# Optimization experiments

Measured on AMD Instinct MI355X. Metric: run time of the kernel, lower is better.

The kernel has to match this reference:

```python
import jax, jax.numpy as jnp
from jax import lax
import numpy as np

B, S, H, L = 128, 256, 768, 24


def setup_inputs() -> dict:
    key = jax.random.key(0)
    k_tf, k_len, k_w, k_tr, k_st, k_en = jax.random.split(key, 6)
    token_features = jax.random.normal(k_tf, (B, S, H), dtype=jnp.float32)
    # contiguous valid lengths in [3, S] (>=3 so that stripping CLS/SEP leaves >=1 token)
    lengths = jax.random.randint(k_len, (B,), 3, S + 1)
    pos = jnp.arange(S)
    input_mask = (pos[None, :] < lengths[:, None]).astype(jnp.int32)
    true_label_mask = (pos[None, :] < (lengths - 2)[:, None]).astype(jnp.int32)
    W = jax.random.normal(k_w, (H, L), dtype=jnp.float32) * 0.02
    b = jnp.zeros((L,), dtype=jnp.float32)
    transitions = jax.random.normal(k_tr, (L, L), dtype=jnp.float32) * 0.1
    start_trans = jax.random.normal(k_st, (L,), dtype=jnp.float32) * 0.1
    end_trans = jax.random.normal(k_en, (L,), dtype=jnp.float32) * 0.1
    return {
        "token_features": token_features,
        "input_mask": input_mask,
        "true_label_mask": true_label_mask,
        "W": W,
        "b": b,
        "transitions": transitions,
        "start_trans": start_trans,
        "end_trans": end_trans,
    }


def _compact(x, mask):
    """Vectorized version of the torch per-token copy loop: for each row,
    gather valid tokens (mask==1) preserving order, drop the first and last
    valid token (CLS/SEP), left-pack into a zero tensor."""
    # stable argsort puts valid positions first, in order
    order = jnp.argsort(1 - mask.astype(jnp.int32), axis=1)  # [B,S]
    gathered = jnp.take_along_axis(x, order[:, :, None], axis=1)  # [B,S,H]
    # drop first valid token (shift left by 1), pad a zero row at the end
    shifted = jnp.concatenate([gathered[:, 1:], jnp.zeros_like(gathered[:, :1])], axis=1)
    n_valid = mask.sum(axis=1)  # [B]
    keep = jnp.arange(x.shape[1])[None, :] < (n_valid[:, None] - 2)  # also drops last (SEP)
    return jnp.where(keep[:, :, None], shifted, 0.0)


def _viterbi(emissions, mask, transitions, start_trans, end_trans):
    """Masked Viterbi decode. emissions [B,S,L], mask [B,S] bool."""
    Bn, Sn, Ln = emissions.shape
    lbl = jnp.arange(Ln)
    score0 = start_trans[None, :] + emissions[:, 0]  # [B,L]

    def step(score, xs):
        em_t, m_t = xs  # [B,L], [B]
        cand = score[:, :, None] + transitions[None]  # [B,prev,curr]
        best = cand.max(axis=1) + em_t
        bp = cand.argmax(axis=1)  # [B,L] best prev tag per curr tag
        new_score = jnp.where(m_t[:, None], best, score)
        bp = jnp.where(m_t[:, None], bp, lbl[None, :])  # identity backpointer on pad
        return new_score, bp

    ems = jnp.swapaxes(emissions[:, 1:], 0, 1)  # [S-1,B,L]
    ms = jnp.swapaxes(mask[:, 1:], 0, 1)  # [S-1,B]
    final, bps = lax.scan(step, score0, (ems, ms))
    final = final + end_trans[None, :]
    best_score = final.max(axis=1)  # [B]
    last_tag = final.argmax(axis=1)  # [B]

    def back(tag, bp):  # tag: tag at time t; bp: bp_t -> tag at t-1
        prev = jnp.take_along_axis(bp, tag[:, None], axis=1)[:, 0]
        return prev, tag

    tag0, tags_rest = lax.scan(back, last_tag, bps, reverse=True)  # tags_rest [S-1,B]
    path = jnp.concatenate([tag0[:, None], jnp.swapaxes(tags_rest, 0, 1)], axis=1)  # [B,S]
    return best_score, path


def reference(token_features, input_mask, true_label_mask, W, b, transitions, start_trans, end_trans):
    mask = input_mask.astype(bool)
    wv = _compact(token_features, mask)  # dropout is identity at inference
    emissions = jax.nn.sigmoid(wv @ W + b)  # [B,S,L]
    _, path = _viterbi(emissions, true_label_mask != 0, transitions, start_trans, end_trans)
    return path
```

## Files before the change

kernel.cpp:

```cpp
#include <hip/hip_runtime.h>
#include <hip/hip_bf16.h>
#include <math.h>

#define NB 128
#define NS 256
#define NH 768
#define NL 24
#define ASTR 68

__global__ __launch_bounds__(256) void ner_emis(
    const float* __restrict__ tf, const int* __restrict__ tlm,
    const float* __restrict__ W, const float* __restrict__ bias,
    float* __restrict__ E)
{
    const int b    = blockIdx.x >> 3;
    const int tile = (blockIdx.x & 7) << 5;
    const int tid  = threadIdx.x;
    if (tlm[b*NS + tile] == 0) return;

    __shared__ float lds[8*32*25];
    float* As = lds;
    float* Ws = lds + 32*ASTR;
    float* Pr = lds;

    const int tok  = tid & 15;
    const int ksub = tid >> 4;
    const int kk   = ksub << 2;
    const int rot  = ksub & 3;

    float acc0[NL], acc1[NL];
    #pragma unroll
    for (int l = 0; l < NL; ++l) { acc0[l] = 0.f; acc1[l] = 0.f; }

    const float* tfb = tf + (size_t)(b*NS)*NH;

    for (int kc0 = 0; kc0 < NH; kc0 += 64) {
        #pragma unroll
        for (int i = 0; i < 2; ++i) {
            int idx  = tid + (i << 8);
            int row  = idx >> 4;
            int c4   = idx & 15;
            int trow = tile + row + 1;
            if (trow > 255) trow = 255;
            float4 v = *(const float4*)(tfb + (size_t)trow*NH + kc0 + (c4 << 2));
            float* dst = As + row*ASTR + (c4 << 2);
            dst[0] = v.x; dst[1] = v.y; dst[2] = v.z; dst[3] = v.w;
        }
        {
            const float4* wsrc = (const float4*)(W + (size_t)kc0*NL);
            float4* wdst = (float4*)Ws;
            for (int i = tid; i < 384; i += 256) wdst[i] = wsrc[i];
        }
        __syncthreads();

        const float* A0 = As + tok*ASTR + kk;
        const float* A1 = A0 + 16*ASTR;
        const float* Wr = Ws + kk*NL;
        #pragma unroll
        for (int s = 0; s < 4; ++s) {
            const int j = (s + rot) & 3;
            float a0 = A0[j];
            float a1 = A1[j];
            const float4* w4 = (const float4*)(Wr + j*NL);
            float wv[NL];
            #pragma unroll
            for (int i = 0; i < 6; ++i) {
                float4 w = w4[i];
                wv[4*i+0] = w.x; wv[4*i+1] = w.y; wv[4*i+2] = w.z; wv[4*i+3] = w.w;
            }
            #pragma unroll
            for (int l = 0; l < NL; ++l) {
                acc0[l] = fmaf(a0, wv[l], acc0[l]);
                acc1[l] = fmaf(a1, wv[l], acc1[l]);
            }
        }
        __syncthreads();
    }

    if (ksub >= 8) {
        float* p = Pr + ((ksub-8)*32 + tok)*25;
        float* q = p + 16*25;
        #pragma unroll
        for (int l = 0; l < NL; ++l) { p[l] = acc0[l]; q[l] = acc1[l]; }
    }
    __syncthreads();
    if (ksub < 8) {
        const float* p = Pr + (ksub*32 + tok)*25;
        const float* q = p + 16*25;
        #pragma unroll
        for (int l = 0; l < NL; ++l) { acc0[l] += p[l]; acc1[l] += q[l]; }
    }
    __syncthreads();
    if (ksub < 8) {
        float* p = Pr + (ksub*32 + tok)*25;
        float* q = p + 16*25;
        #pragma unroll
        for (int l = 0; l < NL; ++l) { p[l] = acc0[l]; q[l] = acc1[l]; }
    }
    __syncthreads();

    const int* tm = tlm + b*NS + tile;
    float* Eb = E + (size_t)(b*NS + tile)*NL;
    #pragma unroll
    for (int i = 0; i < 3; ++i) {
        int o = tid + (i << 8);
        int t = o / NL, l = o % NL;
        if (tm[t]) {
            float s = 0.f;
            #pragma unroll
            for (int ks = 0; ks < 8; ++ks)
                s += Pr[(ks*32 + t)*25 + l];
            float x = s + bias[l];
            Eb[t*NL + l] = 1.0f/(1.0f + expf(-x));
        }
    }
}

__global__ __launch_bounds__(256) void ner_viterbi(
    const float* __restrict__ E, const int* __restrict__ tlm,
    const float* __restrict__ trans, const float* __restrict__ st,
    const float* __restrict__ en, int* __restrict__ out)
{
    const int tid = threadIdx.x;
    const int b   = blockIdx.x;
    const int bS  = b*NS;

    __shared__ float Esh[NS*NL];
    __shared__ float scl[NS*NL];
    __shared__ float Tt[NL*NL];
    __shared__ float fin[NL];
    __shared__ unsigned char tr_s[NL][NS];
    __shared__ int chosen[12];
    __shared__ int nsh, ltag;

    {
        const float4* src = (const float4*)(E + (size_t)bS*NL);
        float4* dst = (float4*)Esh;
        #pragma unroll
        for (int j = 0; j < 6; ++j) dst[tid + (j << 8)] = src[tid + (j << 8)];
    }
    for (int i = tid; i < NL*NL; i += 256) {
        int c = i / NL, p = i % NL;
        Tt[i] = trans[p*NL + c];
    }
    if (tid < 64) {
        int a = tlm[bS+tid] + tlm[bS+tid+64] + tlm[bS+tid+128] + tlm[bS+tid+192];
        #pragma unroll
        for (int off = 32; off > 0; off >>= 1) a += __shfl_down(a, off, 64);
        if (tid == 0) nsh = a;
    }
    __syncthreads();
    const int n = nsh;

    if (tid < 64) {
        const int c = tid % 24;
        float Tc[24];
        #pragma unroll
        for (int p = 0; p < 24; ++p) Tc[p] = trans[p*NL + c];

        auto rl = [](float v, int p) {
            return __int_as_float(__builtin_amdgcn_readlane(__float_as_int(v), p));
        };

        float sv = st[c] + Esh[c];
        scl[c] = sv;
        float scr[24];
        #pragma unroll
        for (int p = 0; p < 24; ++p) scr[p] = rl(sv, p);

        auto step = [&](int t, float em) {
            float cand[24];
            #pragma unroll
            for (int p = 0; p < 24; ++p) cand[p] = scr[p] + Tc[p];
            float m0 = fmaxf(fmaxf(cand[0],  cand[1]),  cand[2]);
            float m1 = fmaxf(fmaxf(cand[3],  cand[4]),  cand[5]);
            float m2 = fmaxf(fmaxf(cand[6],  cand[7]),  cand[8]);
            float m3 = fmaxf(fmaxf(cand[9],  cand[10]), cand[11]);
            float m4 = fmaxf(fmaxf(cand[12], cand[13]), cand[14]);
            float m5 = fmaxf(fmaxf(cand[15], cand[16]), cand[17]);
            float m6 = fmaxf(fmaxf(cand[18], cand[19]), cand[20]);
            float m7 = fmaxf(fmaxf(cand[21], cand[22]), cand[23]);
            float q0 = fmaxf(fmaxf(m0, m1), m2);
            float q1 = fmaxf(fmaxf(m3, m4), m5);
            float q2 = fmaxf(m6, m7);
            float best = fmaxf(fmaxf(q0, q1), q2);
            sv = best + em;
            scl[t*NL + c] = sv;
            #pragma unroll
            for (int p = 0; p < 24; ++p) scr[p] = rl(sv, p);
        };

        int t = 1;
        for (; t + 8 <= n; t += 8) {
            float em[8];
            const float* eb = Esh + t*NL + c;
            #pragma unroll
            for (int j = 0; j < 8; ++j) em[j] = eb[j*NL];
            #pragma unroll
            for (int j = 0; j < 8; ++j) step(t + j, em[j]);
        }
        for (; t < n; ++t) step(t, Esh[t*NL + c]);
        fin[c] = sv + en[c];
    }
    __syncthreads();

    if (tid == 0) {
        float bv = fin[0]; int bt = 0;
        #pragma unroll
        for (int cc = 1; cc < 24; ++cc) { if (fin[cc] > bv) { bv = fin[cc]; bt = cc; } }
        ltag = bt;
    }
    __syncthreads();

    const int K = (n > 1) ? (n - 1 + 9) / 10 : 1;
    if (n > 1 && tid < 240) {
        const int w = tid / 24 + 1, h = tid % 24;
        int tlo = (w-1)*K; if (tlo > n-1) tlo = n-1;
        int thi = w*K;     if (thi > n-1) thi = n-1;
        int cur = h;
        for (int t = thi; t > tlo; --t) {
            const float4* sp = (const float4*)(scl + (t-1)*NL);
            const float4* up = (const float4*)(Tt  + cur*NL);
            float cand[24];
            #pragma unroll
            for (int i = 0; i < 6; ++i) {
                float4 s = sp[i], u = up[i];
                cand[4*i+0] = s.x + u.x;
                cand[4*i+1] = s.y + u.y;
                cand[4*i+2] = s.z + u.z;
                cand[4*i+3] = s.w + u.w;
            }
            float best = cand[0]; int arg = 0;
            #pragma unroll
            for (int p = 1; p < 24; ++p) { if (cand[p] > best) { best = cand[p]; arg = p; } }
            tr_s[h][t-1] = (unsigned char)arg;
            cur = arg;
        }
    }
    __syncthreads();

    if (tid == 0) {
        int cur = ltag;
        for (int w = 10; w >= 1; --w) {
            chosen[w] = cur;
            int tlo = (w-1)*K; if (tlo > n-1) tlo = n-1;
            int thi = w*K;     if (thi > n-1) thi = n-1;
            if (thi > tlo) cur = tr_s[cur][tlo];
        }
    }
    __syncthreads();

    {
        const int t = tid;
        int tag;
        if (t >= n-1) tag = ltag;
        else { int w = t / K + 1; tag = tr_s[chosen[w]][t]; }
        out[bS + t] = tag;
    }
}

extern "C" void kernel_launch(void* const* d_in, const int* in_sizes, int n_in,
                              void* d_out, int out_size, void* d_ws, size_t ws_size,
                              hipStream_t stream) {
    const float* tf    = (const float*)d_in[0];
    const int*   tlm   = (const int*)  d_in[2];
    const float* W     = (const float*)d_in[3];
    const float* bias  = (const float*)d_in[4];
    const float* trans = (const float*)d_in[5];
    const float* st    = (const float*)d_in[6];
    const float* en    = (const float*)d_in[7];
    float* E = (float*)d_ws;

    ner_emis<<<dim3(NB*8), dim3(256), 0, stream>>>(tf, tlm, W, bias, E);
    ner_viterbi<<<dim3(NB), dim3(256), 0, stream>>>(E, tlm, trans, st, en, (int*)d_out);
}
```

Before: 207.5 us.

## Pack two batch rows per wavefront in Viterbi forward pass using ds_bpermute

The Viterbi kernel now handles two batch rows per block, one in each 32-lane half of a single wavefront. Score broadcasts switch from readlane to ds_bpermute, and emissions are prefetched from global memory instead of first being staged into LDS. The backtrace uses 5 windows per row instead of 10, and only 64 blocks are launched. This is meant to halve the number of serial forward recurrences, at the cost of bpermute latency and both rows running to the longer length.

```diff
diff --git a/kernel.cpp b/kernel.cpp
--- a/kernel.cpp
+++ b/kernel.cpp
@@ -7,6 +7,7 @@
 #define NH 768
 #define NL 24
 #define ASTR 68
+#define NW 5
 
 __global__ __launch_bounds__(256) void ner_emis(
     const float* __restrict__ tf, const int* __restrict__ tlm,
@@ -122,56 +123,60 @@
     const float* __restrict__ en, int* __restrict__ out)
 {
     const int tid = threadIdx.x;
-    const int b   = blockIdx.x;
-    const int bS  = b*NS;
-
-    __shared__ float Esh[NS*NL];
-    __shared__ float scl[NS*NL];
+    const int pb  = blockIdx.x;
+
+    __shared__ float scl[2*NS*NL];
     __shared__ float Tt[NL*NL];
-    __shared__ float fin[NL];
-    __shared__ unsigned char tr_s[NL][NS];
-    __shared__ int chosen[12];
-    __shared__ int nsh, ltag;
-
-    {
-        const float4* src = (const float4*)(E + (size_t)bS*NL);
-        float4* dst = (float4*)Esh;
-        #pragma unroll
-        for (int j = 0; j < 6; ++j) dst[tid + (j << 8)] = src[tid + (j << 8)];
-    }
+    __shared__ float fin_s[2*NL];
+    __shared__ unsigned char tr_s[2][NL][NS];
+    __shared__ int chosen_s[2][NW+1];
+    __shared__ int nsh[2], ltag[2];
+
     for (int i = tid; i < NL*NL; i += 256) {
         int c = i / NL, p = i % NL;
         Tt[i] = trans[p*NL + c];
     }
+    if (tid < 128) {
+        const int wv = tid >> 6, ln = tid & 63;
+        const int bb = 2*pb + wv;
+        int a = tlm[bb*NS+ln] + tlm[bb*NS+ln+64] + tlm[bb*NS+ln+128] + tlm[bb*NS+ln+192];
+        #pragma unroll
+        for (int off = 32; off > 0; off >>= 1) a += __shfl_down(a, off, 64);
+        if (ln == 0) nsh[wv] = a;
+    }
+    __syncthreads();
+    const int nA = nsh[0], nB = nsh[1];
+    const int nmax = __builtin_amdgcn_readfirstlane(nA > nB ? nA : nB);
+
     if (tid < 64) {
-        int a = tlm[bS+tid] + tlm[bS+tid+64] + tlm[bS+tid+128] + tlm[bS+tid+192];
-        #pragma unroll
-        for (int off = 32; off > 0; off >>= 1) a += __shfl_down(a, off, 64);
-        if (tid == 0) nsh = a;
-    }
-    __syncthreads();
-    const int n = nsh;
-
-    if (tid < 64) {
-        const int c = tid % 24;
-        float Tc[24];
-        #pragma unroll
-        for (int p = 0; p < 24; ++p) Tc[p] = trans[p*NL + c];
-
-        auto rl = [](float v, int p) {
-            return __int_as_float(__builtin_amdgcn_readlane(__float_as_int(v), p));
+        const int lane  = tid;
+        const int half  = lane >> 5;
+        const int c     = lane & 31;
+        const int cef   = (c < 24) ? c : 23;
+        const bool valid = (c < 24);
+        const int myb   = 2*pb + half;
+        const int hbase = half << 7;
+        const int nh    = half ? nB : nA;
+
+        float Tc[NL];
+        #pragma unroll
+        for (int p = 0; p < NL; ++p) Tc[p] = trans[p*NL + cef];
+
+        const float* Eb = E + (size_t)(myb*NS)*NL + cef;
+        float* sbase = scl + (half*NS)*NL;
+
+        float sv = st[cef] + Eb[0];
+        if (valid) sbase[c] = sv;
+
+        auto bperm = [](int idx, float v) {
+            return __int_as_float(__builtin_amdgcn_ds_bpermute(idx, __float_as_int(v)));
         };
 
-        float sv = st[c] + Esh[c];
-        scl[c] = sv;
-        float scr[24];
-        #pragma unroll
-        for (int p = 0; p < 24; ++p) scr[p] = rl(sv, p);
-
         auto step = [&](int t, float em) {
-            float cand[24];
-            #pragma unroll
-            for (int p = 0; p < 24; ++p) cand[p] = scr[p] + Tc[p];
+            float cand[NL];
+            #pragma unroll
+            for (int p = 0; p < NL; ++p)
+                cand[p] = bperm(hbase + 4*p, sv) + Tc[p];
             float m0 = fmaxf(fmaxf(cand[0],  cand[1]),  cand[2]);
             float m1 = fmaxf(fmaxf(cand[3],  cand[4]),  cand[5]);
             float m2 = fmaxf(fmaxf(cand[6],  cand[7]),  cand[8]);
@@ -184,78 +189,105 @@
             float q1 = fmaxf(fmaxf(m3, m4), m5);
             float q2 = fmaxf(m6, m7);
             float best = fmaxf(fmaxf(q0, q1), q2);
-            sv = best + em;
-            scl[t*NL + c] = sv;
-            #pragma unroll
-            for (int p = 0; p < 24; ++p) scr[p] = rl(sv, p);
+            float nsv = best + em;
+            sv = (t < nh) ? nsv : sv;
+            if (valid) sbase[t*NL + c] = sv;
         };
 
-        int t = 1;
-        for (; t + 8 <= n; t += 8) {
-            float em[8];
-            const float* eb = Esh + t*NL + c;
-            #pragma unroll
-            for (int j = 0; j < 8; ++j) em[j] = eb[j*NL];
-            #pragma unroll
-            for (int j = 0; j < 8; ++j) step(t + j, em[j]);
-        }
-        for (; t < n; ++t) step(t, Esh[t*NL + c]);
-        fin[c] = sv + en[c];
-    }
-    __syncthreads();
-
-    if (tid == 0) {
-        float bv = fin[0]; int bt = 0;
-        #pragma unroll
-        for (int cc = 1; cc < 24; ++cc) { if (fin[cc] > bv) { bv = fin[cc]; bt = cc; } }
-        ltag = bt;
-    }
-    __syncthreads();
-
-    const int K = (n > 1) ? (n - 1 + 9) / 10 : 1;
-    if (n > 1 && tid < 240) {
-        const int w = tid / 24 + 1, h = tid % 24;
-        int tlo = (w-1)*K; if (tlo > n-1) tlo = n-1;
-        int thi = w*K;     if (thi > n-1) thi = n-1;
-        int cur = h;
-        for (int t = thi; t > tlo; --t) {
-            const float4* sp = (const float4*)(scl + (t-1)*NL);
-            const float4* up = (const float4*)(Tt  + cur*NL);
-            float cand[24];
-            #pragma unroll
-            for (int i = 0; i < 6; ++i) {
-                float4 s = sp[i], u = up[i];
-                cand[4*i+0] = s.x + u.x;
-                cand[4*i+1] = s.y + u.y;
-                cand[4*i+2] = s.z + u.z;
-                cand[4*i+3] = s.w + u.w;
-            }
-            float best = cand[0]; int arg = 0;
-            #pragma unroll
-            for (int p = 1; p < 24; ++p) { if (cand[p] > best) { best = cand[p]; arg = p; } }
-            tr_s[h][t-1] = (unsigned char)arg;
-            cur = arg;
-        }
-    }
-    __syncthreads();
-
-    if (tid == 0) {
-        int cur = ltag;
-        for (int w = 10; w >= 1; --w) {
-            chosen[w] = cur;
+        float emb[8];
+        #pragma unroll
+        for (int j = 0; j < 8; ++j) {
+            int tp = 1 + j; if (tp > NS-1) tp = NS-1;
+            emb[j] = Eb[(size_t)tp*NL];
+        }
+        for (int t0 = 1; t0 < nmax; t0 += 8) {
+            float emc[8];
+            #pragma unroll
+            for (int j = 0; j < 8; ++j) emc[j] = emb[j];
+            #pragma unroll
+            for (int j = 0; j < 8; ++j) {
+                int tp = t0 + 8 + j; if (tp > NS-1) tp = NS-1;
+                emb[j] = Eb[(size_t)tp*NL];
+            }
+            #pragma unroll
+            for (int j = 0; j < 8; ++j) {
+                int t = t0 + j;
+                if (t >= nmax) break;
+                step(t, emc[j]);
+            }
+        }
+        if (valid) fin_s[half*NL + c] = sv + en[cef];
+    }
+    __syncthreads();
+
+    if (tid < 2) {
+        const float* f = fin_s + tid*NL;
+        float bv = f[0]; int bt = 0;
+        #pragma unroll
+        for (int cc = 1; cc < 24; ++cc) { if (f[cc] > bv) { bv = f[cc]; bt = cc; } }
+        ltag[tid] = bt;
+    }
+    __syncthreads();
+
+    if (tid < 2*NW*24) {
+        int g = tid;
+        const int bb = g / (NW*24); g -= bb*NW*24;
+        const int w  = g / 24 + 1;
+        const int h  = g % 24;
+        const int n  = nsh[bb];
+        if (n > 1) {
+            const int K = (n - 1 + NW - 1) / NW;
             int tlo = (w-1)*K; if (tlo > n-1) tlo = n-1;
             int thi = w*K;     if (thi > n-1) thi = n-1;
-            if (thi > tlo) cur = tr_s[cur][tlo];
+            const float* sbase = scl + (bb*NS)*NL;
+            int cur = h;
+            for (int t = thi; t > tlo; --t) {
+                const float4* sp = (const float4*)(sbase + (t-1)*NL);
+                const float4* up = (const float4*)(Tt + cur*NL);
+                float cand[NL];
+                #pragma unroll
+                for (int i = 0; i < 6; ++i) {
+                    float4 s = sp[i], u = up[i];
+                    cand[4*i+0] = s.x + u.x;
+                    cand[4*i+1] = s.y + u.y;
+                    cand[4*i+2] = s.z + u.z;
+                    cand[4*i+3] = s.w + u.w;
+                }
+                float best = cand[0]; int arg = 0;
+                #pragma unroll
+                for (int p = 1; p < 24; ++p) { if (cand[p] > best) { best = cand[p]; arg = p; } }
+                tr_s[bb][h][t-1] = (unsigned char)arg;
+                cur = arg;
+            }
+        }
+    }
+    __syncthreads();
+
+    if (tid < 2) {
+        const int bb = tid;
+        const int n  = nsh[bb];
+        const int K  = (n > 1) ? (n - 1 + NW - 1) / NW : 1;
+        int cur = ltag[bb];
+        for (int w = NW; w >= 1; --w) {
+            chosen_s[bb][w] = cur;
+            int tlo = (w-1)*K; if (tlo > n-1) tlo = n-1;
+            int thi = w*K;     if (thi > n-1) thi = n-1;
+            if (thi > tlo) cur = tr_s[bb][cur][tlo];
         }
     }
     __syncthreads();
 
     {
         const int t = tid;
-        int tag;
-        if (t >= n-1) tag = ltag;
-        else { int w = t / K + 1; tag = tr_s[chosen[w]][t]; }
-        out[bS + t] = tag;
+        #pragma unroll
+        for (int bb = 0; bb < 2; ++bb) {
+            const int n = nsh[bb];
+            const int K = (n > 1) ? (n - 1 + NW - 1) / NW : 1;
+            int tag;
+            if (t >= n-1) tag = ltag[bb];
+            else { int w = t / K + 1; tag = tr_s[bb][chosen_s[bb][w]][t]; }
+            out[(2*pb + bb)*NS + t] = tag;
+        }
     }
 }
 
@@ -272,5 +304,5 @@
     float* E = (float*)d_ws;
 
     ner_emis<<<dim3(NB*8), dim3(256), 0, stream>>>(tf, tlm, W, bias, E);
-    ner_viterbi<<<dim3(NB), dim3(256), 0, stream>>>(E, tlm, trans, st, en, (int*)d_out);
+    ner_viterbi<<<dim3(NB/2), dim3(256), 0, stream>>>(E, tlm, trans, st, en, (int*)d_out);
 }
```

Result: slower. 238.9 us (+15.2%).
